# Performance work log

Hardware: AMD Instinct MI355X
Metric: run time of the kernel (lower is better)

Reference implementation:

```python
import jax, jax.numpy as jnp
import numpy as np

VOCAB = 50000
SEQ = 2048
BATCH = 64
D = 256


def setup_inputs() -> dict:
    key = jax.random.key(0)
    ks = jax.random.split(key, 9)
    x = jax.random.randint(ks[0], (SEQ, BATCH), 0, VOCAB)  # token ids, 0 = pad
    emb = jax.random.normal(ks[1], (VOCAB, D), jnp.float32) * 0.02
    emb = emb.at[0].set(0.0)  # padding_idx=0
    idf = jax.random.uniform(ks[2], (VOCAB,), jnp.float32, 0.1, 10.0)
    W1 = jax.random.normal(ks[3], (100, D), jnp.float32) * (1.0 / np.sqrt(D))
    b1 = jax.random.normal(ks[4], (100,), jnp.float32) * 0.01
    W2 = jax.random.normal(ks[5], (150, 100), jnp.float32) * 0.1
    b2 = jax.random.normal(ks[6], (150,), jnp.float32) * 0.01
    W3 = jax.random.normal(ks[7], (2, 150), jnp.float32) * 0.1
    b3 = jax.random.normal(ks[8], (2,), jnp.float32) * 0.01
    return {"x": x, "emb": emb, "idf": idf, "W1": W1, "b1": b1,
            "W2": W2, "b2": b2, "W3": W3, "b3": b3}


def reference(x, emb, idf, W1, b1, W2, b2, W3, b3):
    tokens = x.T  # [B, S] (nums = x.permute(1, 0))
    vocab = emb.shape[0]

    # per-row term frequency: histogram (scatter-add) then gather back
    def tf_row(row):  # row: [S] int
        return jnp.zeros((vocab,), jnp.float32).at[row].add(1.0)[row]

    tf = jax.vmap(tf_row)(tokens)                      # [B, S]
    scores = jnp.where(tokens == 0, 0.0, tf * idf[tokens])  # [B, S]

    # bmm of (B, D, S) with (B, S, 1) == tf-idf weighted sum of embeddings
    pooled = jnp.einsum('bsd,bs->bd', emb[tokens], scores)  # [B, D]

    h = jax.nn.relu(pooled @ W1.T + b1)
    h = jax.nn.relu(h @ W2.T + b2)
    return jax.nn.softmax(h @ W3.T + b3, axis=-1)  # [B, 2]
```

## Files before the change

kernel.cpp:

```cpp
#include <hip/hip_runtime.h>

#define VOCAB 50000
#define SEQ   2048
#define BATCH 64
#define DIM   256
#define NC    16
#define CHUNK (SEQ / NC)
#define H1    100
#define H2    150

__global__ void k_scores(const int* __restrict__ x,
                         const float* __restrict__ idf,
                         float* __restrict__ scores) {
    __shared__ int tok[SEQ];
    const int b = blockIdx.y;
    const int part = blockIdx.x;
    const int t = threadIdx.x;

    for (int s = t; s < SEQ; s += 512)
        tok[s] = x[s * BATCH + b];
    __syncthreads();

    const int p = part * 512 + t;
    const int mytok = tok[p];
    int cnt = 0;
#pragma unroll 8
    for (int i = 0; i < SEQ; ++i)
        cnt += (tok[i] == mytok) ? 1 : 0;

    float sc = (mytok == 0) ? 0.0f : (float)cnt * idf[mytok];
    scores[b * SEQ + p] = sc;
}

__global__ void k_pool(const int* __restrict__ x,
                       const float* __restrict__ emb,
                       const float* __restrict__ scores,
                       float* __restrict__ partials) {
    __shared__ int   tok[CHUNK];
    __shared__ float sc[CHUNK];
    const int c = blockIdx.x;
    const int b = blockIdx.y;
    const int d = threadIdx.x;
    const int s0 = c * CHUNK;

    if (d < CHUNK) {
        tok[d] = x[(s0 + d) * BATCH + b];
        sc[d]  = scores[b * SEQ + s0 + d];
    }
    __syncthreads();

    float acc = 0.0f;
#pragma unroll 4
    for (int i = 0; i < CHUNK; ++i) {
        const float* row = emb + (size_t)tok[i] * DIM;
        acc = fmaf(row[d], sc[i], acc);
    }
    partials[((size_t)c * BATCH + b) * DIM + d] = acc;
}

__global__ void k_mlp(const float* __restrict__ partials,
                      const float* __restrict__ W1, const float* __restrict__ b1,
                      const float* __restrict__ W2, const float* __restrict__ b2,
                      const float* __restrict__ W3, const float* __restrict__ b3,
                      float* __restrict__ out) {
    __shared__ float pld[DIM];
    __shared__ float h1[H1];
    __shared__ float h2[H2];
    __shared__ float logit[2];
    const int b = blockIdx.x;
    const int t = threadIdx.x;

    float acc = 0.0f;
#pragma unroll
    for (int c = 0; c < NC; ++c)
        acc += partials[((size_t)c * BATCH + b) * DIM + t];
    pld[t] = acc;
    __syncthreads();

    if (t < H1) {
        float a = b1[t];
        const float* w = W1 + t * DIM;
#pragma unroll 4
        for (int k = 0; k < DIM; ++k) a = fmaf(pld[k], w[k], a);
        h1[t] = fmaxf(a, 0.0f);
    }
    __syncthreads();

    if (t < H2) {
        float a = b2[t];
        const float* w = W2 + t * H1;
#pragma unroll 4
        for (int k = 0; k < H1; ++k) a = fmaf(h1[k], w[k], a);
        h2[t] = fmaxf(a, 0.0f);
    }
    __syncthreads();

    if (t < 2) {
        float a = b3[t];
        const float* w = W3 + t * H2;
#pragma unroll 4
        for (int k = 0; k < H2; ++k) a = fmaf(h2[k], w[k], a);
        logit[t] = a;
    }
    __syncthreads();

    if (t == 0) {
        float m  = fmaxf(logit[0], logit[1]);
        float e0 = expf(logit[0] - m);
        float e1 = expf(logit[1] - m);
        float inv = 1.0f / (e0 + e1);
        out[b * 2 + 0] = e0 * inv;
        out[b * 2 + 1] = e1 * inv;
    }
}

extern "C" void kernel_launch(void* const* d_in, const int* in_sizes, int n_in,
                              void* d_out, int out_size, void* d_ws, size_t ws_size,
                              hipStream_t stream) {
    const int*   x   = (const int*)  d_in[0];
    const float* emb = (const float*)d_in[1];
    const float* idf = (const float*)d_in[2];
    const float* W1  = (const float*)d_in[3];
    const float* b1  = (const float*)d_in[4];
    const float* W2  = (const float*)d_in[5];
    const float* b2  = (const float*)d_in[6];
    const float* W3  = (const float*)d_in[7];
    const float* b3  = (const float*)d_in[8];
    float* out = (float*)d_out;

    float* scores   = (float*)d_ws;
    float* partials = scores + (size_t)BATCH * SEQ;

    k_scores<<<dim3(4, BATCH), 512, 0, stream>>>(x, idf, scores);
    k_pool  <<<dim3(NC, BATCH), DIM, 0, stream>>>(x, emb, scores, partials);
    k_mlp   <<<BATCH, DIM, 0, stream>>>(partials, W1, b1, W2, b2, W3, b3, out);
}
```

Before: 158.8 us.

## Replace quadratic token counting with shared-memory hash histogram and vectorize pool/MLP

After: 158.4 us. Within noise of the previous version (-0.3%).

```diff
diff --git a/kernel.cpp b/kernel.cpp
--- a/kernel.cpp
+++ b/kernel.cpp
@@ -8,107 +8,139 @@
 #define CHUNK (SEQ / NC)
 #define H1    100
 #define H2    150
+#define HASH  4096
 
-__global__ void k_scores(const int* __restrict__ x,
-                         const float* __restrict__ idf,
-                         float* __restrict__ scores) {
-    __shared__ int tok[SEQ];
-    const int b = blockIdx.y;
-    const int part = blockIdx.x;
+__global__ __launch_bounds__(1024)
+void k_scores(const int* __restrict__ x,
+              const float* __restrict__ idf,
+              float* __restrict__ scores) {
+    __shared__ int   tok[SEQ];
+    __shared__ int   hkey[HASH];
+    __shared__ int   hcnt[HASH];
+    const int b = blockIdx.x;
     const int t = threadIdx.x;
 
-    for (int s = t; s < SEQ; s += 512)
-        tok[s] = x[s * BATCH + b];
+    for (int i = t; i < HASH; i += 1024) { hkey[i] = -1; hcnt[i] = 0; }
+    for (int s = t; s < SEQ; s += 1024)  tok[s] = x[s * BATCH + b];
     __syncthreads();
 
-    const int p = part * 512 + t;
-    const int mytok = tok[p];
-    int cnt = 0;
-#pragma unroll 8
-    for (int i = 0; i < SEQ; ++i)
-        cnt += (tok[i] == mytok) ? 1 : 0;
-
-    float sc = (mytok == 0) ? 0.0f : (float)cnt * idf[mytok];
-    scores[b * SEQ + p] = sc;
-}
-
-__global__ void k_pool(const int* __restrict__ x,
-                       const float* __restrict__ emb,
-                       const float* __restrict__ scores,
-                       float* __restrict__ partials) {
-    __shared__ int   tok[CHUNK];
-    __shared__ float sc[CHUNK];
-    const int c = blockIdx.x;
-    const int b = blockIdx.y;
-    const int d = threadIdx.x;
-    const int s0 = c * CHUNK;
-
-    if (d < CHUNK) {
-        tok[d] = x[(s0 + d) * BATCH + b];
-        sc[d]  = scores[b * SEQ + s0 + d];
+    for (int s = t; s < SEQ; s += 1024) {
+        const int mytok = tok[s];
+        unsigned h = ((unsigned)mytok * 2654435761u) >> 20;
+        while (true) {
+            int prev = atomicCAS(&hkey[h], -1, mytok);
+            if (prev == -1 || prev == mytok) { atomicAdd(&hcnt[h], 1); break; }
+            h = (h + 1) & (HASH - 1);
+        }
     }
     __syncthreads();
 
-    float acc = 0.0f;
-#pragma unroll 4
-    for (int i = 0; i < CHUNK; ++i) {
-        const float* row = emb + (size_t)tok[i] * DIM;
-        acc = fmaf(row[d], sc[i], acc);
+    for (int s = t; s < SEQ; s += 1024) {
+        const int mytok = tok[s];
+        unsigned h = ((unsigned)mytok * 2654435761u) >> 20;
+        while (hkey[h] != mytok) h = (h + 1) & (HASH - 1);
+        float sc = (mytok == 0) ? 0.0f : (float)hcnt[h] * idf[mytok];
+        scores[b * SEQ + s] = sc;
     }
-    partials[((size_t)c * BATCH + b) * DIM + d] = acc;
 }
 
-__global__ void k_mlp(const float* __restrict__ partials,
-                      const float* __restrict__ W1, const float* __restrict__ b1,
-                      const float* __restrict__ W2, const float* __restrict__ b2,
-                      const float* __restrict__ W3, const float* __restrict__ b3,
-                      float* __restrict__ out) {
+__global__ __launch_bounds__(256)
+void k_pool(const int* __restrict__ x,
+            const float* __restrict__ emb,
+            const float* __restrict__ scores,
+            float* __restrict__ partials) {
+    __shared__ int   tok[CHUNK];
+    __shared__ float sc[CHUNK];
+    __shared__ float acc_lds[4][DIM];
+    const int c = blockIdx.x;
+    const int b = blockIdx.y;
+    const int t = threadIdx.x;
+    const int wave = t >> 6, lane = t & 63;
+    const int s0 = c * CHUNK;
+
+    if (t < CHUNK) {
+        tok[t] = x[(s0 + t) * BATCH + b];
+        sc[t]  = scores[b * SEQ + s0 + t];
+    }
+    __syncthreads();
+
+    float4 acc = make_float4(0.f, 0.f, 0.f, 0.f);
+    for (int i = wave; i < CHUNK; i += 4) {
+        const float s = sc[i];
+        const float4 v = ((const float4*)(emb + (size_t)tok[i] * DIM))[lane];
+        acc.x = fmaf(v.x, s, acc.x);
+        acc.y = fmaf(v.y, s, acc.y);
+        acc.z = fmaf(v.z, s, acc.z);
+        acc.w = fmaf(v.w, s, acc.w);
+    }
+    ((float4*)acc_lds[wave])[lane] = acc;
+    __syncthreads();
+
+    if (t < DIM) {
+        float r = acc_lds[0][t] + acc_lds[1][t] + acc_lds[2][t] + acc_lds[3][t];
+        partials[((size_t)c * BATCH + b) * DIM + t] = r;
+    }
+}
+
+__global__ __launch_bounds__(256)
+void k_mlp(const float* __restrict__ partials,
+           const float* __restrict__ W1, const float* __restrict__ b1,
+           const float* __restrict__ W2, const float* __restrict__ b2,
+           const float* __restrict__ W3, const float* __restrict__ b3,
+           float* __restrict__ out) {
     __shared__ float pld[DIM];
-    __shared__ float h1[H1];
-    __shared__ float h2[H2];
+    __shared__ float h1[112];
+    __shared__ float h2[152];
     __shared__ float logit[2];
     const int b = blockIdx.x;
     const int t = threadIdx.x;
+    const int wave = t >> 6, lane = t & 63;
 
-    float acc = 0.0f;
+    float a = 0.0f;
 #pragma unroll
     for (int c = 0; c < NC; ++c)
-        acc += partials[((size_t)c * BATCH + b) * DIM + t];
-    pld[t] = acc;
+        a += partials[((size_t)c * BATCH + b) * DIM + t];
+    pld[t] = a;
     __syncthreads();
 
-    if (t < H1) {
-        float a = b1[t];
-        const float* w = W1 + t * DIM;
-#pragma unroll 4
-        for (int k = 0; k < DIM; ++k) a = fmaf(pld[k], w[k], a);
-        h1[t] = fmaxf(a, 0.0f);
+    for (int j = wave; j < H1; j += 4) {
+        const float4 wv = ((const float4*)(W1 + j * DIM))[lane];
+        const float4 pv = ((const float4*)pld)[lane];
+        float d = wv.x * pv.x + wv.y * pv.y + wv.z * pv.z + wv.w * pv.w;
+#pragma unroll
+        for (int off = 32; off; off >>= 1) d += __shfl_down(d, off);
+        if (lane == 0) h1[j] = fmaxf(d + b1[j], 0.0f);
     }
     __syncthreads();
 
-    if (t < H2) {
-        float a = b2[t];
-        const float* w = W2 + t * H1;
-#pragma unroll 4
-        for (int k = 0; k < H1; ++k) a = fmaf(h1[k], w[k], a);
-        h2[t] = fmaxf(a, 0.0f);
+    for (int j = wave; j < H2; j += 4) {
+        float d = 0.0f;
+        if (lane < 25) {
+            const float4 wv = ((const float4*)(W2 + j * H1))[lane];
+            const float4 hv = ((const float4*)h1)[lane];
+            d = wv.x * hv.x + wv.y * hv.y + wv.z * hv.z + wv.w * hv.w;
+        }
+#pragma unroll
+        for (int off = 32; off; off >>= 1) d += __shfl_down(d, off);
+        if (lane == 0) h2[j] = fmaxf(d + b2[j], 0.0f);
     }
     __syncthreads();
 
-    if (t < 2) {
-        float a = b3[t];
-        const float* w = W3 + t * H2;
-#pragma unroll 4
-        for (int k = 0; k < H2; ++k) a = fmaf(h2[k], w[k], a);
-        logit[t] = a;
+    if (wave < 2) {
+        const int j = wave;
+        float d = 0.0f;
+        for (int k = lane; k < H2; k += 64) d += W3[j * H2 + k] * h2[k];
+#pragma unroll
+        for (int off = 32; off; off >>= 1) d += __shfl_down(d, off);
+        if (lane == 0) logit[j] = d + b3[j];
     }
     __syncthreads();
 
     if (t == 0) {
-        float m  = fmaxf(logit[0], logit[1]);
-        float e0 = expf(logit[0] - m);
-        float e1 = expf(logit[1] - m);
-        float inv = 1.0f / (e0 + e1);
+        const float m  = fmaxf(logit[0], logit[1]);
+        const float e0 = __expf(logit[0] - m);
+        const float e1 = __expf(logit[1] - m);
+        const float inv = 1.0f / (e0 + e1);
         out[b * 2 + 0] = e0 * inv;
         out[b * 2 + 1] = e1 * inv;
     }
@@ -131,7 +163,7 @@
     float* scores   = (float*)d_ws;
     float* partials = scores + (size_t)BATCH * SEQ;
 
-    k_scores<<<dim3(4, BATCH), 512, 0, stream>>>(x, idf, scores);
-    k_pool  <<<dim3(NC, BATCH), DIM, 0, stream>>>(x, emb, scores, partials);
-    k_mlp   <<<BATCH, DIM, 0, stream>>>(partials, W1, b1, W2, b2, W3, b3, out);
+    k_scores<<<BATCH, 1024, 0, stream>>>(x, idf, scores);
+    k_pool  <<<dim3(NC, BATCH), 256, 0, stream>>>(x, emb, scores, partials);
+    k_mlp   <<<BATCH, 256, 0, stream>>>(partials, W1, b1, W2, b2, W3, b3, out);
 }
```
